# Kernel tuning notes

Hardware: AMD Instinct MI355X
Metric: run time of the kernel (lower is better)

The kernel has to match this reference:

```python
import jax, jax.numpy as jnp
import numpy as np

NEG = -10000.0

def _wn(W, g):
    # weight_norm with dim=None: single scalar g scaling W / ||W||_F
    return g * W / jnp.linalg.norm(W)

def setup_inputs() -> dict:
    key = jax.random.key(0)
    ks = jax.random.split(key, 10)
    B, N, H, P = 128, 4096, 128, 128
    v = jax.random.normal(ks[0], (B, N, H), jnp.float32)
    q = jax.random.normal(ks[1], (B, H), jnp.float32)
    mask = jnp.ones((B, N), jnp.float32)
    # params (out_dim, in_dim) like torch Linear
    Wv = jax.random.normal(ks[2], (P, H), jnp.float32) / np.sqrt(H)
    bv = jnp.zeros((P,), jnp.float32)
    gv = jnp.float32(jnp.linalg.norm(Wv))
    Wq = jax.random.normal(ks[3], (P, H), jnp.float32) / np.sqrt(H)
    bq = jnp.zeros((P,), jnp.float32)
    gq = jnp.float32(jnp.linalg.norm(Wq))
    Wa = jax.random.normal(ks[4], (1, P), jnp.float32) / np.sqrt(P)
    ba = jnp.zeros((1,), jnp.float32)
    ga = jnp.float32(jnp.linalg.norm(Wa))
    return {"v": v, "q": q, "mask": mask, "Wv": Wv, "bv": bv, "gv": gv,
            "Wq": Wq, "bq": bq, "gq": gq, "Wa": Wa, "ba": ba, "ga": ga}

def reference(v, q, mask, Wv, bv, gv, Wq, bq, gq, Wa, ba, ga):
    # FCNet projections (dropout is identity at inference; FCNet applies no relu)
    v_proj = jnp.einsum('bnh,ph->bnp', v, _wn(Wv, gv)) + bv        # [B,N,P]
    q_proj = (q @ _wn(Wq, gq).T + bq)[:, None, :]                   # [B,1,P]
    h = jax.nn.relu(v_proj + q_proj)                                # [B,N,P]
    logits = jnp.einsum('bnp,p->bn', h, _wn(Wa, ga)[0]) + ba[0]     # [B,N]
    logits = logits + (1.0 - mask) * NEG
    w = jax.nn.softmax(logits, axis=-1)                             # [B,N]
    w_att = w[:, :, None]                                           # [B,N,1]
    att = jnp.sum(v * w_att, axis=1)                                # [B,H]
    return att, w_att
```

## Files before the change

kernel.cpp:

```cpp
#include <hip/hip_runtime.h>

typedef _Float16 half8_t __attribute__((ext_vector_type(8)));
typedef float f32x4 __attribute__((ext_vector_type(4)));

#define B_ 128
#define N_ 4096
#define H_ 128
#define P_ 128
#define CCH 16
#define ROWS_PER_CHUNK (N_ / CCH)
#define TILE 64
#define TILES (ROWS_PER_CHUNK / TILE)

#define OFF_SCALES 0
#define OFF_WA     16
#define OFF_QPC    256
#define OFF_BPACK  16640
#define OFF_LOGITS 24832
#define OFF_PART   549120
#define OFF_FIN    819456

__device__ __forceinline__ float block_reduce_sum(float val, float* red, int tid) {
    red[tid] = val;
    __syncthreads();
    for (int s = 128; s > 0; s >>= 1) {
        if (tid < s) red[tid] += red[tid + s];
        __syncthreads();
    }
    float r = red[0];
    __syncthreads();
    return r;
}

__global__ __launch_bounds__(256) void k0a_prep(
    const float* __restrict__ Wv, const float* __restrict__ gv,
    const float* __restrict__ Wq, const float* __restrict__ gq,
    const float* __restrict__ Wa, const float* __restrict__ ga,
    float* __restrict__ ws)
{
    __shared__ float red[256];
    __shared__ float s_sv, s_sa;
    const int tid = threadIdx.x;

    float sv2 = 0.f, sq2 = 0.f, sa2 = 0.f;
    for (int i = tid; i < P_ * H_; i += 256) {
        float x = Wv[i]; sv2 += x * x;
        float y = Wq[i]; sq2 += y * y;
    }
    if (tid < P_) { float z = Wa[tid]; sa2 = z * z; }

    float nv2 = block_reduce_sum(sv2, red, tid);
    float nq2 = block_reduce_sum(sq2, red, tid);
    float na2 = block_reduce_sum(sa2, red, tid);

    if (tid == 0) {
        float sv = gv[0] / sqrtf(nv2);
        float sq = gq[0] / sqrtf(nq2);
        float sa = ga[0] / sqrtf(na2);
        ws[OFF_SCALES + 0] = sv;
        ws[OFF_SCALES + 1] = sq;
        ws[OFF_SCALES + 2] = sa;
        s_sv = sv; s_sa = sa;
    }
    __syncthreads();

    const float sv = s_sv, sa = s_sa;
    _Float16* bp = (_Float16*)(ws + OFF_BPACK);
    for (int s = tid; s < 16384; s += 256) {
        int j  = s & 7;
        int L  = (s >> 3) & 63;
        int pt = (s >> 9) & 7;
        int kk = s >> 12;
        int p = pt * 16 + (L & 15);
        int h = kk * 32 + (L >> 4) * 8 + j;
        bp[s] = (_Float16)(Wv[p * H_ + h] * sv);
    }
    if (tid < P_) ws[OFF_WA + tid] = Wa[tid] * sa;
}

__global__ __launch_bounds__(128) void k0b_qproj(
    const float* __restrict__ q, const float* __restrict__ Wq,
    const float* __restrict__ bq, const float* __restrict__ bv,
    float* __restrict__ ws)
{
    const int b = blockIdx.x, p = threadIdx.x;
    const float sq = ws[OFF_SCALES + 1];
    const float* qr = q + b * H_;
    const float* wr = Wq + p * H_;
    float acc = 0.f;
#pragma unroll 8
    for (int h = 0; h < H_; ++h) acc += qr[h] * wr[h];
    ws[OFF_QPC + b * P_ + p] = acc * sq + bq[p] + bv[p];
}

__global__ __launch_bounds__(256) void k1_main(
    const float* __restrict__ v, const float* __restrict__ mask,
    const float* __restrict__ ba, float* __restrict__ ws)
{
    const int c = blockIdx.x;
    const int b = blockIdx.y;
    const int tid = threadIdx.x;
    const int lane = tid & 63;
    const int w = tid >> 6;

    __shared__ __align__(16) _Float16 Bl[16384];
    __shared__ float qpcs[P_];
    __shared__ float was[P_];
    __shared__ float lgbuf[TILE];
    __shared__ float wbuf[TILE];
    __shared__ float sc[4];
    __shared__ float oredu[256 * 4];

    {
        const uint4* src = (const uint4*)(ws + OFF_BPACK);
        uint4* dst = (uint4*)Bl;
#pragma unroll
        for (int i = 0; i < 8; ++i) dst[tid + i * 256] = src[tid + i * 256];
        if (tid < P_) {
            qpcs[tid] = ws[OFF_QPC + b * P_ + tid];
            was[tid]  = ws[OFF_WA + tid];
        }
        if (tid == 0) { sc[0] = -1e30f; sc[1] = 0.f; sc[2] = 0.f; }
    }
    float o4[4] = {0.f, 0.f, 0.f, 0.f};
    const float ba0 = ba[0];
    __syncthreads();

    const int h4 = (tid & 31) * 4;
    const int rs = tid >> 5;

    for (int it = 0; it < TILES; ++it) {
        const int n0 = c * ROWS_PER_CHUNK + it * TILE;

        const int arow = n0 + w * 16 + (lane & 15);
        const int colb = (lane >> 4) * 8;
        const float* vrow = v + ((size_t)b * N_ + arow) * H_;
        half8_t af[4];
#pragma unroll
        for (int kk = 0; kk < 4; ++kk) {
            const float4* p4 = (const float4*)(vrow + kk * 32 + colb);
            float4 f0 = p4[0], f1 = p4[1];
            half8_t a;
            a[0] = (_Float16)f0.x; a[1] = (_Float16)f0.y;
            a[2] = (_Float16)f0.z; a[3] = (_Float16)f0.w;
            a[4] = (_Float16)f1.x; a[5] = (_Float16)f1.y;
            a[6] = (_Float16)f1.z; a[7] = (_Float16)f1.w;
            af[kk] = a;
        }
        float lp[4] = {0.f, 0.f, 0.f, 0.f};
        const int pcol = lane & 15;
#pragma unroll
        for (int pt = 0; pt < 8; ++pt) {
            f32x4 acc = {0.f, 0.f, 0.f, 0.f};
#pragma unroll
            for (int kk = 0; kk < 4; ++kk) {
                half8_t bf = *(const half8_t*)&Bl[(((kk * 8 + pt) * 64) + lane) * 8];
                acc = __builtin_amdgcn_mfma_f32_16x16x32_f16(af[kk], bf, acc, 0, 0, 0);
            }
            const int p = pt * 16 + pcol;
            const float qv = qpcs[p];
            const float wv = was[p];
#pragma unroll
            for (int r = 0; r < 4; ++r)
                lp[r] += fmaxf(acc[r] + qv, 0.f) * wv;
        }
#pragma unroll
        for (int m = 1; m <= 8; m <<= 1) {
#pragma unroll
            for (int r = 0; r < 4; ++r)
                lp[r] += __shfl_xor(lp[r], m, 64);
        }
        if ((lane & 15) == 0) {
#pragma unroll
            for (int r = 0; r < 4; ++r)
                lgbuf[w * 16 + (lane >> 4) * 4 + r] = lp[r];
        }
        __syncthreads();

        if (w == 0) {
            const int r = lane;
            const int n = n0 + r;
            float lg = lgbuf[r] + ba0 + (1.0f - mask[b * N_ + n]) * (-10000.0f);
            ws[OFF_LOGITS + (size_t)b * N_ + n] = lg;
            float mt = lg;
#pragma unroll
            for (int m = 1; m <= 32; m <<= 1) mt = fmaxf(mt, __shfl_xor(mt, m, 64));
            const float m_old = sc[0];
            const float m_new = fmaxf(m_old, mt);
            const float alpha = __expf(m_old - m_new);
            const float wr = __expf(lg - m_new);
            wbuf[r] = wr;
            float s = wr;
#pragma unroll
            for (int m = 1; m <= 32; m <<= 1) s += __shfl_xor(s, m, 64);
            if (lane == 0) {
                sc[1] = sc[1] * alpha + s;
                sc[0] = m_new;
                sc[2] = alpha;
            }
        }
        __syncthreads();

        const float alpha = sc[2];
#pragma unroll
        for (int qq = 0; qq < 4; ++qq) o4[qq] *= alpha;
#pragma unroll
        for (int k = 0; k < 8; ++k) {
            const int r = rs * 8 + k;
            const float wr = wbuf[r];
            const float4 vv = *(const float4*)(v + ((size_t)b * N_ + n0 + r) * H_ + h4);
            o4[0] += wr * vv.x; o4[1] += wr * vv.y;
            o4[2] += wr * vv.z; o4[3] += wr * vv.w;
        }
    }

    __syncthreads();
#pragma unroll
    for (int qq = 0; qq < 4; ++qq) oredu[tid * 4 + qq] = o4[qq];
    __syncthreads();

    float* part = ws + OFF_PART + ((size_t)b * CCH + c) * 132;
    if (tid < 32) {
        float s0 = 0.f, s1 = 0.f, s2 = 0.f, s3 = 0.f;
#pragma unroll
        for (int g = 0; g < 8; ++g) {
            const int bi = (g * 32 + tid) * 4;
            s0 += oredu[bi]; s1 += oredu[bi + 1];
            s2 += oredu[bi + 2]; s3 += oredu[bi + 3];
        }
        const int h = tid * 4;
        part[2 + h] = s0; part[2 + h + 1] = s1;
        part[2 + h + 2] = s2; part[2 + h + 3] = s3;
    }
    if (tid == 0) { part[0] = sc[0]; part[1] = sc[1]; }
}

__global__ __launch_bounds__(128) void k2a_combine(
    float* __restrict__ ws, float* __restrict__ out)
{
    const int b = blockIdx.x, h = threadIdx.x;
    const float* part = ws + OFF_PART + (size_t)b * CCH * 132;
    float m = -1e30f;
#pragma unroll
    for (int c = 0; c < CCH; ++c) m = fmaxf(m, part[c * 132]);
    float l = 0.f, a = 0.f;
#pragma unroll
    for (int c = 0; c < CCH; ++c) {
        const float e = __expf(part[c * 132] - m);
        l += e * part[c * 132 + 1];
        a += e * part[c * 132 + 2 + h];
    }
    out[b * H_ + h] = a / l;
    if (h == 0) {
        ws[OFF_FIN + b] = m;
        ws[OFF_FIN + B_ + b] = 1.0f / l;
    }
}

__global__ __launch_bounds__(256) void k2b_weights(
    const float* __restrict__ ws, float* __restrict__ out)
{
    const int idx = blockIdx.x * 256 + threadIdx.x;
    const int b = idx >> 12;
    const float lg = ws[OFF_LOGITS + idx];
    out[B_ * H_ + idx] = __expf(lg - ws[OFF_FIN + b]) * ws[OFF_FIN + B_ + b];
}

extern "C" void kernel_launch(void* const* d_in, const int* in_sizes, int n_in,
                              void* d_out, int out_size, void* d_ws, size_t ws_size,
                              hipStream_t stream) {
    const float* v    = (const float*)d_in[0];
    const float* q    = (const float*)d_in[1];
    const float* mask = (const float*)d_in[2];
    const float* Wv   = (const float*)d_in[3];
    const float* bv   = (const float*)d_in[4];
    const float* gv   = (const float*)d_in[5];
    const float* Wq   = (const float*)d_in[6];
    const float* bq   = (const float*)d_in[7];
    const float* gq   = (const float*)d_in[8];
    const float* Wa   = (const float*)d_in[9];
    const float* ba   = (const float*)d_in[10];
    const float* ga   = (const float*)d_in[11];
    float* out = (float*)d_out;
    float* ws  = (float*)d_ws;

    k0a_prep<<<1, 256, 0, stream>>>(Wv, gv, Wq, gq, Wa, ga, ws);
    k0b_qproj<<<B_, 128, 0, stream>>>(q, Wq, bq, bv, ws);
    k1_main<<<dim3(CCH, B_), 256, 0, stream>>>(v, mask, ba, ws);
    k2a_combine<<<B_, 128, 0, stream>>>(ws, out);
    k2b_weights<<<(B_ * N_) / 256, 256, 0, stream>>>(ws, out);
}
```

Baseline: 434.8 us.

## Keep v rows in registers and run per-wave online softmax without block syncs

Each wave now keeps the fp32 v values it loads for the MFMA A-operand in registers and reuses them for the weighted sum. This removes the second global read of v. Softmax state is tracked per wave with shuffles instead of through shared memory, so the two __syncthreads per tile are gone. The four wave states are merged at the end through shared memory, and q_proj is folded into the MFMA accumulator init. The cost is much higher register use (o32 and vf arrays) under a launch-bounds hint of 4 blocks, plus a 32-wide shuffle reduction at the end.

```diff
diff --git a/kernel.cpp b/kernel.cpp
--- a/kernel.cpp
+++ b/kernel.cpp
@@ -9,8 +9,7 @@
 #define P_ 128
 #define CCH 16
 #define ROWS_PER_CHUNK (N_ / CCH)
-#define TILE 64
-#define TILES (ROWS_PER_CHUNK / TILE)
+#define TILES 4
 
 #define OFF_SCALES 0
 #define OFF_WA     16
@@ -93,7 +92,7 @@
     ws[OFF_QPC + b * P_ + p] = acc * sq + bq[p] + bv[p];
 }
 
-__global__ __launch_bounds__(256) void k1_main(
+__global__ __launch_bounds__(256, 4) void k1_main(
     const float* __restrict__ v, const float* __restrict__ mask,
     const float* __restrict__ ba, float* __restrict__ ws)
 {
@@ -106,10 +105,8 @@
     __shared__ __align__(16) _Float16 Bl[16384];
     __shared__ float qpcs[P_];
     __shared__ float was[P_];
-    __shared__ float lgbuf[TILE];
-    __shared__ float wbuf[TILE];
-    __shared__ float sc[4];
-    __shared__ float oredu[256 * 4];
+    __shared__ float obuf[4][P_];
+    __shared__ float mbuf[4], lbuf[4];
 
     {
         const uint4* src = (const uint4*)(ws + OFF_BPACK);
@@ -120,26 +117,33 @@
             qpcs[tid] = ws[OFF_QPC + b * P_ + tid];
             was[tid]  = ws[OFF_WA + tid];
         }
-        if (tid == 0) { sc[0] = -1e30f; sc[1] = 0.f; sc[2] = 0.f; }
-    }
-    float o4[4] = {0.f, 0.f, 0.f, 0.f};
+    }
     const float ba0 = ba[0];
     __syncthreads();
 
-    const int h4 = (tid & 31) * 4;
-    const int rs = tid >> 5;
+    const int rloc = lane & 15;
+    const int grp  = lane >> 4;
+    const int colb = grp * 8;
+
+    float m_w = -1e30f, l_w = 0.f;
+    float o32[32];
+#pragma unroll
+    for (int j = 0; j < 32; ++j) o32[j] = 0.f;
 
     for (int it = 0; it < TILES; ++it) {
-        const int n0 = c * ROWS_PER_CHUNK + it * TILE;
-
-        const int arow = n0 + w * 16 + (lane & 15);
-        const int colb = (lane >> 4) * 8;
-        const float* vrow = v + ((size_t)b * N_ + arow) * H_;
+        const int n0w = c * ROWS_PER_CHUNK + it * 64 + w * 16;
+
+        const float* vrow = v + ((size_t)b * N_ + n0w + rloc) * H_;
+        float vf[32];
         half8_t af[4];
 #pragma unroll
         for (int kk = 0; kk < 4; ++kk) {
             const float4* p4 = (const float4*)(vrow + kk * 32 + colb);
             float4 f0 = p4[0], f1 = p4[1];
+            vf[kk * 8 + 0] = f0.x; vf[kk * 8 + 1] = f0.y;
+            vf[kk * 8 + 2] = f0.z; vf[kk * 8 + 3] = f0.w;
+            vf[kk * 8 + 4] = f1.x; vf[kk * 8 + 5] = f1.y;
+            vf[kk * 8 + 6] = f1.z; vf[kk * 8 + 7] = f1.w;
             half8_t a;
             a[0] = (_Float16)f0.x; a[1] = (_Float16)f0.y;
             a[2] = (_Float16)f0.z; a[3] = (_Float16)f0.w;
@@ -147,92 +151,100 @@
             a[6] = (_Float16)f1.z; a[7] = (_Float16)f1.w;
             af[kk] = a;
         }
-        float lp[4] = {0.f, 0.f, 0.f, 0.f};
-        const int pcol = lane & 15;
-#pragma unroll
-        for (int pt = 0; pt < 8; ++pt) {
-            f32x4 acc = {0.f, 0.f, 0.f, 0.f};
-#pragma unroll
-            for (int kk = 0; kk < 4; ++kk) {
-                half8_t bf = *(const half8_t*)&Bl[(((kk * 8 + pt) * 64) + lane) * 8];
-                acc = __builtin_amdgcn_mfma_f32_16x16x32_f16(af[kk], bf, acc, 0, 0, 0);
+
+        float lp[4];
+        {
+            const float qv0 = qpcs[rloc];
+            lp[0] = lp[1] = lp[2] = lp[3] = 0.f;
+#pragma unroll
+            for (int pt = 0; pt < 8; ++pt) {
+                const int p = pt * 16 + rloc;
+                const float qv = qpcs[p];
+                f32x4 acc = {qv, qv, qv, qv};
+#pragma unroll
+                for (int kk = 0; kk < 4; ++kk) {
+                    half8_t bf = *(const half8_t*)&Bl[(((kk * 8 + pt) * 64) + lane) * 8];
+                    acc = __builtin_amdgcn_mfma_f32_16x16x32_f16(af[kk], bf, acc, 0, 0, 0);
+                }
+                const float wv = was[p];
+#pragma unroll
+                for (int r = 0; r < 4; ++r)
+                    lp[r] += fmaxf(acc[r], 0.f) * wv;
             }
-            const int p = pt * 16 + pcol;
-            const float qv = qpcs[p];
-            const float wv = was[p];
-#pragma unroll
-            for (int r = 0; r < 4; ++r)
-                lp[r] += fmaxf(acc[r] + qv, 0.f) * wv;
+            (void)qv0;
         }
 #pragma unroll
         for (int m = 1; m <= 8; m <<= 1) {
 #pragma unroll
-            for (int r = 0; r < 4; ++r)
-                lp[r] += __shfl_xor(lp[r], m, 64);
-        }
-        if ((lane & 15) == 0) {
-#pragma unroll
-            for (int r = 0; r < 4; ++r)
-                lgbuf[w * 16 + (lane >> 4) * 4 + r] = lp[r];
-        }
-        __syncthreads();
-
-        if (w == 0) {
-            const int r = lane;
-            const int n = n0 + r;
-            float lg = lgbuf[r] + ba0 + (1.0f - mask[b * N_ + n]) * (-10000.0f);
-            ws[OFF_LOGITS + (size_t)b * N_ + n] = lg;
-            float mt = lg;
-#pragma unroll
-            for (int m = 1; m <= 32; m <<= 1) mt = fmaxf(mt, __shfl_xor(mt, m, 64));
-            const float m_old = sc[0];
-            const float m_new = fmaxf(m_old, mt);
-            const float alpha = __expf(m_old - m_new);
-            const float wr = __expf(lg - m_new);
-            wbuf[r] = wr;
-            float s = wr;
-#pragma unroll
-            for (int m = 1; m <= 32; m <<= 1) s += __shfl_xor(s, m, 64);
-            if (lane == 0) {
-                sc[1] = sc[1] * alpha + s;
-                sc[0] = m_new;
-                sc[2] = alpha;
-            }
-        }
-        __syncthreads();
-
-        const float alpha = sc[2];
-#pragma unroll
-        for (int qq = 0; qq < 4; ++qq) o4[qq] *= alpha;
-#pragma unroll
-        for (int k = 0; k < 8; ++k) {
-            const int r = rs * 8 + k;
-            const float wr = wbuf[r];
-            const float4 vv = *(const float4*)(v + ((size_t)b * N_ + n0 + r) * H_ + h4);
-            o4[0] += wr * vv.x; o4[1] += wr * vv.y;
-            o4[2] += wr * vv.z; o4[3] += wr * vv.w;
-        }
-    }
-
-    __syncthreads();
-#pragma unroll
-    for (int qq = 0; qq < 4; ++qq) oredu[tid * 4 + qq] = o4[qq];
+            for (int r = 0; r < 4; ++r) lp[r] += __shfl_xor(lp[r], m, 64);
+        }
+#pragma unroll
+        for (int r = 0; r < 4; ++r) {
+            const float mk = mask[(size_t)b * N_ + n0w + grp * 4 + r];
+            lp[r] += ba0 + (1.0f - mk) * (-10000.0f);
+        }
+
+        const int srcl = (rloc >> 2) << 4;
+        float t0 = __shfl(lp[0], srcl, 64);
+        float t1 = __shfl(lp[1], srcl, 64);
+        float t2 = __shfl(lp[2], srcl, 64);
+        float t3 = __shfl(lp[3], srcl, 64);
+        float a01 = (rloc & 1) ? t1 : t0;
+        float a23 = (rloc & 1) ? t3 : t2;
+        float lg_me = (rloc & 2) ? a23 : a01;
+
+        if (lane < 16) ws[OFF_LOGITS + (size_t)b * N_ + n0w + lane] = lg_me;
+
+        float mt = fmaxf(fmaxf(lp[0], lp[1]), fmaxf(lp[2], lp[3]));
+        mt = fmaxf(mt, __shfl_xor(mt, 16, 64));
+        mt = fmaxf(mt, __shfl_xor(mt, 32, 64));
+
+        const float mn = fmaxf(m_w, mt);
+        const float alpha = __expf(m_w - mn);
+        const float wme = __expf(lg_me - mn);
+        float s = wme;
+#pragma unroll
+        for (int m = 1; m <= 8; m <<= 1) s += __shfl_xor(s, m, 64);
+        l_w = l_w * alpha + s;
+        m_w = mn;
+
+        if (alpha != 1.0f) {
+#pragma unroll
+            for (int j = 0; j < 32; ++j) o32[j] *= alpha;
+        }
+#pragma unroll
+        for (int j = 0; j < 32; ++j) o32[j] += wme * vf[j];
+    }
+
+#pragma unroll
+    for (int m = 1; m <= 8; m <<= 1) {
+#pragma unroll
+        for (int j = 0; j < 32; ++j) o32[j] += __shfl_xor(o32[j], m, 64);
+    }
+    {
+        const int j0 = rloc * 2;
+#pragma unroll
+        for (int u = 0; u < 2; ++u) {
+            const int j = j0 + u;
+            obuf[w][(j >> 3) * 32 + colb + (j & 7)] = o32[j];
+        }
+        if (lane == 0) { mbuf[w] = m_w; lbuf[w] = l_w; }
+    }
     __syncthreads();
 
     float* part = ws + OFF_PART + ((size_t)b * CCH + c) * 132;
-    if (tid < 32) {
-        float s0 = 0.f, s1 = 0.f, s2 = 0.f, s3 = 0.f;
-#pragma unroll
-        for (int g = 0; g < 8; ++g) {
-            const int bi = (g * 32 + tid) * 4;
-            s0 += oredu[bi]; s1 += oredu[bi + 1];
-            s2 += oredu[bi + 2]; s3 += oredu[bi + 3];
-        }
-        const int h = tid * 4;
-        part[2 + h] = s0; part[2 + h + 1] = s1;
-        part[2 + h + 2] = s2; part[2 + h + 3] = s3;
-    }
-    if (tid == 0) { part[0] = sc[0]; part[1] = sc[1]; }
+    if (tid < P_) {
+        const float mb = fmaxf(fmaxf(mbuf[0], mbuf[1]), fmaxf(mbuf[2], mbuf[3]));
+        float lb = 0.f, oh = 0.f;
+#pragma unroll
+        for (int ww = 0; ww < 4; ++ww) {
+            const float e = __expf(mbuf[ww] - mb);
+            lb += e * lbuf[ww];
+            oh += e * obuf[ww][tid];
+        }
+        part[2 + tid] = oh;
+        if (tid == 0) { part[0] = mb; part[1] = lb; }
+    }
 }
 
 __global__ __launch_bounds__(128) void k2a_combine(
```

New measurement: 679.6 us. +56.3%, slower.
